# Optimization experiments

Measured on AMD Instinct MI355X. Metric: run time of the kernel, lower is better.

The kernel has to match this reference:

```python
import jax, jax.numpy as jnp
import numpy as np

EPS = float(np.finfo(np.float32).eps)

_base_x = np.array([[-1, 0, 1], [-2, 0, 2], [-1, 0, 1]], dtype=np.float32)
# 3D Sobel kernels (as in the torch module)
SOBEL_X_3D = np.stack([_base_x, 2 * _base_x, _base_x], axis=0)            # d-axis replication, x-grad along last axis
SOBEL_Y_3D = np.transpose(SOBEL_X_3D, (0, 2, 1))                          # rows/cols swapped -> y-grad
SOBEL_Z_3D = np.transpose(SOBEL_X_3D, (2, 1, 0))                          # z-grad along depth axis
# verify against explicit tensors from the source
assert np.array_equal(SOBEL_Y_3D[0], np.array([[-1, -2, -1], [0, 0, 0], [1, 2, 1]], dtype=np.float32))
assert np.array_equal(SOBEL_Z_3D[0], np.array([[-1, -2, -1], [-2, -4, -2], [-1, -2, -1]], dtype=np.float32))


def _sobel3d(image, kernel_np):
    # image: [B,1,D,H,W]; kernel: [3,3,3] -> OIDHW [1,1,3,3,3]
    k = jnp.asarray(kernel_np).reshape(1, 1, 3, 3, 3)
    return jax.lax.conv_general_dilated(
        image, k, window_strides=(1, 1, 1), padding='SAME',
        dimension_numbers=('NCDHW', 'OIDHW', 'NCDHW'))


def _normalized_gradient(image, mask, eta):
    # image, mask: [B,1,D,H,W]
    gx = _sobel3d(image, SOBEL_X_3D)
    gy = _sobel3d(image, SOBEL_Y_3D)
    gz = _sobel3d(image, SOBEL_Z_3D)
    grad = jnp.concatenate([gx, gy, gz], axis=1)          # [B,3,D,H,W]
    sq = jnp.sum(grad * grad, axis=1)                     # [B,D,H,W]
    norm = jnp.sqrt(sq + EPS)
    m = mask[:, 0]                                        # squeeze channel -> [B,D,H,W]
    dims = (1, 2, 3)
    auto_eps = eta / jnp.sum(m, axis=dims) * jnp.sum(norm * m, axis=dims)  # [B]
    auto_eps = auto_eps.reshape(-1, 1, 1, 1)
    denom = jnp.sqrt(sq + auto_eps ** 2 + EPS)            # [B,D,H,W]
    return grad / denom[:, None]                          # [B,3,D,H,W]


def setup_inputs() -> dict:
    key = jax.random.key(0)
    k1, k2 = jax.random.split(key)
    shape = (2, 1, 160, 160, 160)
    pred = jax.random.normal(k1, shape, dtype=jnp.float32)
    target = jax.random.normal(k2, shape, dtype=jnp.float32)
    mask = jnp.ones(shape, dtype=jnp.float32)
    return {"pred": pred, "target": target, "mask": mask}


def reference(pred, target, mask):
    eta = 1.0
    fixed_grad = jax.lax.stop_gradient(_normalized_gradient(target, mask, eta))
    warped_grad = _normalized_gradient(pred, mask, eta)
    inner = jnp.sum(fixed_grad * warped_grad, axis=1)     # [B,D,H,W]
    return 1.0 - jnp.mean(inner ** 2)
```

## Files before the change

kernel.cpp:

```cpp
#include <hip/hip_runtime.h>
#include <math.h>

#define DIM 160
#define NB 2
#define CHUNK 5
#define NCHZ (DIM / CHUNK)
#define NTHREADS 256
#define EPS_F 1.1920928955078125e-07f


__device__ __forceinline__ float4 ldv(const float* __restrict__ p, bool ok) {
  float4 r = make_float4(0.f, 0.f, 0.f, 0.f);
  if (ok) r = *(const float4*)p;
  return r;
}

__device__ __forceinline__ void plane_P(const float* __restrict__ img, int off0,
                                        bool zok, bool ym, bool yp, bool xl, bool xr,
                                        float (&P1)[4], float (&P2)[4], float (&P3)[4]) {
#pragma unroll
  for (int r = 0; r < 3; ++r) {
    const bool rv = zok && (r == 0 ? ym : (r == 2 ? yp : true));
    const int offr = off0 + (r - 1) * DIM;
    float4 L = ldv(img + offr - 4, rv && xl);
    float4 M = ldv(img + offr, rv);
    float4 R = ldv(img + offr + 4, rv && xr);
    float fm1 = L.w, f0 = M.x, f1 = M.y, f2 = M.z, f3 = M.w, f4 = R.x;
    float S[4], D[4];
    S[0] = fm1 + 2.f * f0 + f1;  D[0] = f1 - fm1;
    S[1] = f0 + 2.f * f1 + f2;   D[1] = f2 - f0;
    S[2] = f1 + 2.f * f2 + f3;   D[2] = f3 - f1;
    S[3] = f2 + 2.f * f3 + f4;   D[3] = f4 - f2;
    if (r == 0) {
#pragma unroll
      for (int j = 0; j < 4; ++j) { P1[j] = D[j]; P2[j] = -S[j]; P3[j] = S[j]; }
    } else if (r == 1) {
#pragma unroll
      for (int j = 0; j < 4; ++j) { P1[j] += 2.f * D[j]; P3[j] += 2.f * S[j]; }
    } else {
#pragma unroll
      for (int j = 0; j < 4; ++j) { P1[j] += D[j]; P2[j] += S[j]; P3[j] += S[j]; }
    }
  }
}

__global__ __launch_bounds__(NTHREADS)
void pass1_kernel(const float* __restrict__ pred, const float* __restrict__ tgt,
                  const float* __restrict__ mask, double* __restrict__ ws) {
  __shared__ float red[2][4];
  const int tid = threadIdx.x;
  const int tx = tid & 7, ty = tid >> 3;
  int bz = blockIdx.z;
  const int im = bz & 1; bz >>= 1;
  const int n = bz / NCHZ;
  const int zs = (bz % NCHZ) * CHUNK;
  const int xb = blockIdx.x * 32 + tx * 4;
  const int y = blockIdx.y * 32 + ty;
  const size_t base = (size_t)n * DIM * DIM * DIM;
  const float* img = (im == 0 ? pred : tgt) + base;
  const float* mb = mask + base;

  const bool xl = (xb >= 4), xr = (xb + 4 < DIM);
  const bool ym = (y >= 1), yp = (y <= DIM - 2);

  float OUT[2][3][4];
#pragma unroll
  for (int s = 0; s < 2; ++s)
#pragma unroll
    for (int f = 0; f < 3; ++f)
#pragma unroll
      for (int j = 0; j < 4; ++j) OUT[s][f][j] = 0.f;

  float am = 0.f, an = 0.f;

#pragma unroll
  for (int i = 0; i < CHUNK + 2; ++i) {
    const int z = zs - 1 + i;
    const bool zok = ((unsigned)z < DIM);
    const int off0 = (z * DIM + y) * DIM + xb;
    float P1[4], P2[4], P3[4];
    plane_P(img, off0, zok, ym, yp, xl, xr, P1, P2, P3);
    const int sA = i & 1, sB = sA ^ 1;
    if (i >= 2) {
      const int zo = z - 1;
      if (im == 0) {
        const float4 mv = *(const float4*)(mb + (zo * DIM + y) * DIM + xb);
        const float m4[4] = {mv.x, mv.y, mv.z, mv.w};
#pragma unroll
        for (int j = 0; j < 4; ++j) {
          float gx = OUT[sA][0][j] + P1[j];
          float gy = OUT[sA][1][j] + P2[j];
          float gz = OUT[sA][2][j] + P3[j];
          am += m4[j];
          an += sqrtf(gx * gx + gy * gy + gz * gz + EPS_F) * m4[j];
        }
      } else {
#pragma unroll
        for (int j = 0; j < 4; ++j) {
          float gx = OUT[sA][0][j] + P1[j];
          float gy = OUT[sA][1][j] + P2[j];
          float gz = OUT[sA][2][j] + P3[j];
          an += sqrtf(gx * gx + gy * gy + gz * gz + EPS_F);
        }
      }
    }
#pragma unroll
    for (int j = 0; j < 4; ++j) {
      OUT[sA][0][j] = P1[j];
      OUT[sA][1][j] = P2[j];
      OUT[sA][2][j] = -P3[j];
      OUT[sB][0][j] += 2.f * P1[j];
      OUT[sB][1][j] += 2.f * P2[j];
    }
  }

  float v0 = am, v1 = an;
#pragma unroll
  for (int off = 32; off > 0; off >>= 1) {
    v0 += __shfl_down(v0, off, 64);
    v1 += __shfl_down(v1, off, 64);
  }
  const int lane = tid & 63, wave = tid >> 6;
  if (lane == 0) { red[0][wave] = v0; red[1][wave] = v1; }
  __syncthreads();
  if (tid == 0) {
    if (im == 0) atomicAdd(&ws[0 + n], (double)(red[0][0] + red[0][1] + red[0][2] + red[0][3]));
    atomicAdd(&ws[2 + 2 * im + n], (double)(red[1][0] + red[1][1] + red[1][2] + red[1][3]));
  }
}

__global__ void compute_c_kernel(double* __restrict__ ws) {
  if (threadIdx.x == 0 && blockIdx.x == 0) {
    for (int n = 0; n < NB; ++n) {
      double inv_m = 1.0 / ws[0 + n];
      double ae_p = ws[2 + n] * inv_m;
      double ae_t = ws[4 + n] * inv_m;
      ws[8 + n] = ae_p * ae_p + (double)EPS_F;
      ws[10 + n] = ae_t * ae_t + (double)EPS_F;
    }
  }
}

__global__ __launch_bounds__(NTHREADS)
void pass2_kernel(const float* __restrict__ pred, const float* __restrict__ tgt,
                  double* __restrict__ ws) {
  __shared__ float red[4];
  const int tid = threadIdx.x;
  const int tx = tid & 7, ty = tid >> 3;
  const int bz = blockIdx.z;
  const int n = bz / NCHZ;
  const int zs = (bz % NCHZ) * CHUNK;
  const int xb = blockIdx.x * 32 + tx * 4;
  const int y = blockIdx.y * 32 + ty;
  const size_t base = (size_t)n * DIM * DIM * DIM;
  const float* pb = pred + base;
  const float* tb = tgt + base;

  const float cp = (float)ws[8 + n];
  const float ct = (float)ws[10 + n];

  const bool xl = (xb >= 4), xr = (xb + 4 < DIM);
  const bool ym = (y >= 1), yp = (y <= DIM - 2);

  float OUT[2][2][3][4];
#pragma unroll
  for (int s = 0; s < 2; ++s)
#pragma unroll
    for (int g = 0; g < 2; ++g)
#pragma unroll
      for (int f = 0; f < 3; ++f)
#pragma unroll
        for (int j = 0; j < 4; ++j) OUT[s][g][f][j] = 0.f;

  float acc = 0.f;

#pragma unroll
  for (int i = 0; i < CHUNK + 2; ++i) {
    const int z = zs - 1 + i;
    const bool zok = ((unsigned)z < DIM);
    const int off0 = (z * DIM + y) * DIM + xb;
    float P[2][3][4];
    plane_P(pb, off0, zok, ym, yp, xl, xr, P[0][0], P[0][1], P[0][2]);
    plane_P(tb, off0, zok, ym, yp, xl, xr, P[1][0], P[1][1], P[1][2]);
    const int sA = i & 1, sB = sA ^ 1;
    if (i >= 2) {
#pragma unroll
      for (int j = 0; j < 4; ++j) {
        float gpx = OUT[sA][0][0][j] + P[0][0][j];
        float gpy = OUT[sA][0][1][j] + P[0][1][j];
        float gpz = OUT[sA][0][2][j] + P[0][2][j];
        float gtx = OUT[sA][1][0][j] + P[1][0][j];
        float gty = OUT[sA][1][1][j] + P[1][1][j];
        float gtz = OUT[sA][1][2][j] + P[1][2][j];
        float sqp = gpx * gpx + gpy * gpy + gpz * gpz;
        float sqt = gtx * gtx + gty * gty + gtz * gtz;
        float dot = gpx * gtx + gpy * gty + gpz * gtz;
        float inner = dot * rsqrtf((sqp + cp) * (sqt + ct));
        acc += inner * inner;
      }
    }
#pragma unroll
    for (int g = 0; g < 2; ++g)
#pragma unroll
      for (int j = 0; j < 4; ++j) {
        OUT[sA][g][0][j] = P[g][0][j];
        OUT[sA][g][1][j] = P[g][1][j];
        OUT[sA][g][2][j] = -P[g][2][j];
        OUT[sB][g][0][j] += 2.f * P[g][0][j];
        OUT[sB][g][1][j] += 2.f * P[g][1][j];
      }
  }

#pragma unroll
  for (int off = 32; off > 0; off >>= 1) acc += __shfl_down(acc, off, 64);
  const int lane = tid & 63, wave = tid >> 6;
  if (lane == 0) red[wave] = acc;
  __syncthreads();
  if (tid == 0) atomicAdd(&ws[6], (double)(red[0] + red[1] + red[2] + red[3]));
}

__global__ void finalize_kernel(const double* __restrict__ ws, float* __restrict__ out) {
  if (threadIdx.x == 0 && blockIdx.x == 0) {
    double mean = ws[6] / ((double)NB * DIM * DIM * DIM);
    out[0] = (float)(1.0 - mean);
  }
}

extern "C" void kernel_launch(void* const* d_in, const int* in_sizes, int n_in,
                              void* d_out, int out_size, void* d_ws, size_t ws_size,
                              hipStream_t stream) {
  const float* pred = (const float*)d_in[0];
  const float* tgt = (const float*)d_in[1];
  const float* mask = (const float*)d_in[2];
  float* out = (float*)d_out;
  double* ws = (double*)d_ws;

  hipMemsetAsync(d_ws, 0, 16 * sizeof(double), stream);

  dim3 grid1(DIM / 32, DIM / 32, NCHZ * NB * 2);
  pass1_kernel<<<grid1, NTHREADS, 0, stream>>>(pred, tgt, mask, ws);
  compute_c_kernel<<<1, 64, 0, stream>>>(ws);
  dim3 grid2(DIM / 32, DIM / 32, NCHZ * NB);
  pass2_kernel<<<grid2, NTHREADS, 0, stream>>>(pred, tgt, ws);
  finalize_kernel<<<1, 64, 0, stream>>>(ws, out);
}
```

Measured before the change: 152.2 us.

## Stage z-planes through double-buffered LDS and fuse pred/target in pass1

Both passes now cooperatively load each z-plane tile with halo (34 rows by 44 floats, for pred and target) into a double-buffered shared-memory buffer, and compute the Sobel stencils from LDS instead of issuing nine overlapping global vector loads per thread. Boundary handling moves from predicated loads to clamped addresses plus multiplicative zero factors. Pass1 processes pred and target in the same block rather than in separate blocks, the z chunk doubles to 10, and the launch bounds request two blocks per CU. The aim is less redundant global/L2 traffic, at the cost of two barriers per plane, more registers and fewer blocks in the grid.

```diff
diff --git a/kernel.cpp b/kernel.cpp
--- a/kernel.cpp
+++ b/kernel.cpp
@@ -3,38 +3,83 @@
 
 #define DIM 160
 #define NB 2
-#define CHUNK 5
+#define CHUNK 10
 #define NCHZ (DIM / CHUNK)
 #define NTHREADS 256
 #define EPS_F 1.1920928955078125e-07f
 
-
-__device__ __forceinline__ float4 ldv(const float* __restrict__ p, bool ok) {
-  float4 r = make_float4(0.f, 0.f, 0.f, 0.f);
-  if (ok) r = *(const float4*)p;
-  return r;
-}
-
-__device__ __forceinline__ void plane_P(const float* __restrict__ img, int off0,
-                                        bool zok, bool ym, bool yp, bool xl, bool xr,
-                                        float (&P1)[4], float (&P2)[4], float (&P3)[4]) {
-#pragma unroll
-  for (int r = 0; r < 3; ++r) {
-    const bool rv = zok && (r == 0 ? ym : (r == 2 ? yp : true));
-    const int offr = off0 + (r - 1) * DIM;
-    float4 L = ldv(img + offr - 4, rv && xl);
-    float4 M = ldv(img + offr, rv);
-    float4 R = ldv(img + offr + 4, rv && xr);
-    float fm1 = L.w, f0 = M.x, f1 = M.y, f2 = M.z, f3 = M.w, f4 = R.x;
+#define CW 10
+#define RH 34
+#define LS 44
+#define PLANE_F (RH * LS)
+#define NCK (2 * RH * CW)
+
+typedef float v4f __attribute__((ext_vector_type(4)));
+
+__device__ __forceinline__ int imin(int a, int b) { return a < b ? a : b; }
+__device__ __forceinline__ int imax(int a, int b) { return a > b ? a : b; }
+
+
+struct Slot {
+  const float* srcb;
+  int ldsoff;
+  bool act;
+};
+
+__device__ __forceinline__ void make_slots(const float* __restrict__ pb,
+                                           const float* __restrict__ tb,
+                                           int x0, int y0, int tid, Slot (&sl)[3]) {
+#pragma unroll
+  for (int s = 0; s < 3; ++s) {
+    const int i = tid + NTHREADS * s;
+    sl[s].act = (i < NCK);
+    const int ii = sl[s].act ? i : 0;
+    const int img = ii / (RH * CW);
+    const int rem = ii - img * (RH * CW);
+    const int row = rem / CW, ch = rem - row * CW;
+    const int yc = imin(imax(y0 - 1 + row, 0), DIM - 1);
+    const int xc = imin(imax(x0 - 4 + 4 * ch, 0), DIM - 4);
+    sl[s].srcb = (img ? tb : pb) + yc * DIM + xc;
+    sl[s].ldsoff = img * PLANE_F + row * LS + 4 * ch;
+  }
+}
+
+__device__ __forceinline__ void stage_load(const Slot (&sl)[3], int z, v4f (&r)[3]) {
+  const int zoff = imin(imax(z, 0), DIM - 1) * DIM * DIM;
+#pragma unroll
+  for (int s = 0; s < 3; ++s)
+    if (sl[s].act) r[s] = *(const v4f*)(sl[s].srcb + zoff);
+}
+
+__device__ __forceinline__ void stage_write(float* __restrict__ buf,
+                                            const Slot (&sl)[3], const v4f (&r)[3]) {
+#pragma unroll
+  for (int s = 0; s < 3; ++s)
+    if (sl[s].act) *(v4f*)(buf + sl[s].ldsoff) = r[s];
+}
+
+__device__ __forceinline__ void compute_P_lds(const float* __restrict__ pl,
+                                              int tx, int ty,
+                                              float rf0, float rf1, float rf2,
+                                              float fxl, float fxr,
+                                              float (&P1)[4], float (&P2)[4], float (&P3)[4]) {
+#pragma unroll
+  for (int rr = 0; rr < 3; ++rr) {
+    const float rf = (rr == 0) ? rf0 : (rr == 1) ? rf1 : rf2;
+    const float* row = pl + (ty + rr) * LS + 4 * tx;
+    const v4f L = *(const v4f*)row;
+    const v4f M = *(const v4f*)(row + 4);
+    const v4f R = *(const v4f*)(row + 8);
+    const float fm1 = L.w * fxl, f0 = M.x, f1 = M.y, f2 = M.z, f3 = M.w, f4 = R.x * fxr;
     float S[4], D[4];
-    S[0] = fm1 + 2.f * f0 + f1;  D[0] = f1 - fm1;
-    S[1] = f0 + 2.f * f1 + f2;   D[1] = f2 - f0;
-    S[2] = f1 + 2.f * f2 + f3;   D[2] = f3 - f1;
-    S[3] = f2 + 2.f * f3 + f4;   D[3] = f4 - f2;
-    if (r == 0) {
+    S[0] = (fm1 + 2.f * f0 + f1) * rf;  D[0] = (f1 - fm1) * rf;
+    S[1] = (f0 + 2.f * f1 + f2) * rf;   D[1] = (f2 - f0) * rf;
+    S[2] = (f1 + 2.f * f2 + f3) * rf;   D[2] = (f3 - f1) * rf;
+    S[3] = (f2 + 2.f * f3 + f4) * rf;   D[3] = (f4 - f2) * rf;
+    if (rr == 0) {
 #pragma unroll
       for (int j = 0; j < 4; ++j) { P1[j] = D[j]; P2[j] = -S[j]; P3[j] = S[j]; }
-    } else if (r == 1) {
+    } else if (rr == 1) {
 #pragma unroll
       for (int j = 0; j < 4; ++j) { P1[j] += 2.f * D[j]; P3[j] += 2.f * S[j]; }
     } else {
@@ -44,88 +89,110 @@
   }
 }
 
-__global__ __launch_bounds__(NTHREADS)
+__global__ __launch_bounds__(NTHREADS, 2)
 void pass1_kernel(const float* __restrict__ pred, const float* __restrict__ tgt,
                   const float* __restrict__ mask, double* __restrict__ ws) {
-  __shared__ float red[2][4];
+  __shared__ float lds[2][2 * PLANE_F];
+  __shared__ float red[3][4];
   const int tid = threadIdx.x;
   const int tx = tid & 7, ty = tid >> 3;
-  int bz = blockIdx.z;
-  const int im = bz & 1; bz >>= 1;
-  const int n = bz / NCHZ;
-  const int zs = (bz % NCHZ) * CHUNK;
-  const int xb = blockIdx.x * 32 + tx * 4;
-  const int y = blockIdx.y * 32 + ty;
+  const int n = blockIdx.z / NCHZ;
+  const int zs = (blockIdx.z % NCHZ) * CHUNK;
+  const int x0 = blockIdx.x * 32, y0 = blockIdx.y * 32;
   const size_t base = (size_t)n * DIM * DIM * DIM;
-  const float* img = (im == 0 ? pred : tgt) + base;
+  const float* pb = pred + base;
+  const float* tb = tgt + base;
   const float* mb = mask + base;
-
-  const bool xl = (xb >= 4), xr = (xb + 4 < DIM);
-  const bool ym = (y >= 1), yp = (y <= DIM - 2);
-
-  float OUT[2][3][4];
+  const int x = x0 + 4 * tx, y = y0 + ty;
+
+  const float fxl = (x > 0) ? 1.f : 0.f;
+  const float fxr = (x + 4 < DIM) ? 1.f : 0.f;
+  const float fym = (y > 0) ? 1.f : 0.f;
+  const float fyp = (y < DIM - 1) ? 1.f : 0.f;
+
+  Slot sl[3];
+  make_slots(pb, tb, x0, y0, tid, sl);
+
+  float OUT[2][2][3][4];
 #pragma unroll
   for (int s = 0; s < 2; ++s)
 #pragma unroll
-    for (int f = 0; f < 3; ++f)
-#pragma unroll
-      for (int j = 0; j < 4; ++j) OUT[s][f][j] = 0.f;
-
-  float am = 0.f, an = 0.f;
-
-#pragma unroll
-  for (int i = 0; i < CHUNK + 2; ++i) {
+    for (int g = 0; g < 2; ++g)
+#pragma unroll
+      for (int f = 0; f < 3; ++f)
+#pragma unroll
+        for (int j = 0; j < 4; ++j) OUT[s][g][f][j] = 0.f;
+
+  float am = 0.f, anp = 0.f, ant = 0.f;
+  v4f stg[3];
+
+  stage_load(sl, zs - 1, stg);
+  stage_write(lds[0], sl, stg);
+  __syncthreads();
+
+#pragma unroll
+  for (int i = 0; i <= CHUNK + 1; ++i) {
     const int z = zs - 1 + i;
-    const bool zok = ((unsigned)z < DIM);
-    const int off0 = (z * DIM + y) * DIM + xb;
-    float P1[4], P2[4], P3[4];
-    plane_P(img, off0, zok, ym, yp, xl, xr, P1, P2, P3);
+    if (i <= CHUNK) stage_load(sl, zs + i, stg);
+
+    const float fz = ((unsigned)z < DIM) ? 1.f : 0.f;
+    const float* bufb = lds[i & 1];
+    float P[2][3][4];
+    compute_P_lds(bufb, tx, ty, fz * fym, fz, fz * fyp, fxl, fxr,
+                  P[0][0], P[0][1], P[0][2]);
+    compute_P_lds(bufb + PLANE_F, tx, ty, fz * fym, fz, fz * fyp, fxl, fxr,
+                  P[1][0], P[1][1], P[1][2]);
+
     const int sA = i & 1, sB = sA ^ 1;
     if (i >= 2) {
       const int zo = z - 1;
-      if (im == 0) {
-        const float4 mv = *(const float4*)(mb + (zo * DIM + y) * DIM + xb);
-        const float m4[4] = {mv.x, mv.y, mv.z, mv.w};
-#pragma unroll
-        for (int j = 0; j < 4; ++j) {
-          float gx = OUT[sA][0][j] + P1[j];
-          float gy = OUT[sA][1][j] + P2[j];
-          float gz = OUT[sA][2][j] + P3[j];
-          am += m4[j];
-          an += sqrtf(gx * gx + gy * gy + gz * gz + EPS_F) * m4[j];
-        }
-      } else {
-#pragma unroll
-        for (int j = 0; j < 4; ++j) {
-          float gx = OUT[sA][0][j] + P1[j];
-          float gy = OUT[sA][1][j] + P2[j];
-          float gz = OUT[sA][2][j] + P3[j];
-          an += sqrtf(gx * gx + gy * gy + gz * gz + EPS_F);
-        }
+      const v4f mv = *(const v4f*)(mb + (zo * DIM + y) * DIM + x);
+#pragma unroll
+      for (int j = 0; j < 4; ++j) {
+        const float mj = (j == 0) ? mv.x : (j == 1) ? mv.y : (j == 2) ? mv.z : mv.w;
+        float gpx = OUT[sA][0][0][j] + P[0][0][j];
+        float gpy = OUT[sA][0][1][j] + P[0][1][j];
+        float gpz = OUT[sA][0][2][j] + P[0][2][j];
+        float gtx = OUT[sA][1][0][j] + P[1][0][j];
+        float gty = OUT[sA][1][1][j] + P[1][1][j];
+        float gtz = OUT[sA][1][2][j] + P[1][2][j];
+        am += mj;
+        anp += sqrtf(gpx * gpx + gpy * gpy + gpz * gpz + EPS_F) * mj;
+        ant += sqrtf(gtx * gtx + gty * gty + gtz * gtz + EPS_F) * mj;
       }
     }
 #pragma unroll
-    for (int j = 0; j < 4; ++j) {
-      OUT[sA][0][j] = P1[j];
-      OUT[sA][1][j] = P2[j];
-      OUT[sA][2][j] = -P3[j];
-      OUT[sB][0][j] += 2.f * P1[j];
-      OUT[sB][1][j] += 2.f * P2[j];
-    }
-  }
-
-  float v0 = am, v1 = an;
+    for (int g = 0; g < 2; ++g)
+#pragma unroll
+      for (int j = 0; j < 4; ++j) {
+        OUT[sA][g][0][j] = P[g][0][j];
+        OUT[sA][g][1][j] = P[g][1][j];
+        OUT[sA][g][2][j] = -P[g][2][j];
+        OUT[sB][g][0][j] += 2.f * P[g][0][j];
+        OUT[sB][g][1][j] += 2.f * P[g][1][j];
+      }
+
+    if (i <= CHUNK) {
+      __syncthreads();
+      stage_write(lds[(i & 1) ^ 1], sl, stg);
+      __syncthreads();
+    }
+  }
+
+  float v0 = am, v1 = anp, v2 = ant;
 #pragma unroll
   for (int off = 32; off > 0; off >>= 1) {
     v0 += __shfl_down(v0, off, 64);
     v1 += __shfl_down(v1, off, 64);
+    v2 += __shfl_down(v2, off, 64);
   }
   const int lane = tid & 63, wave = tid >> 6;
-  if (lane == 0) { red[0][wave] = v0; red[1][wave] = v1; }
+  if (lane == 0) { red[0][wave] = v0; red[1][wave] = v1; red[2][wave] = v2; }
   __syncthreads();
   if (tid == 0) {
-    if (im == 0) atomicAdd(&ws[0 + n], (double)(red[0][0] + red[0][1] + red[0][2] + red[0][3]));
-    atomicAdd(&ws[2 + 2 * im + n], (double)(red[1][0] + red[1][1] + red[1][2] + red[1][3]));
+    atomicAdd(&ws[0 + n], (double)(red[0][0] + red[0][1] + red[0][2] + red[0][3]));
+    atomicAdd(&ws[2 + n], (double)(red[1][0] + red[1][1] + red[1][2] + red[1][3]));
+    atomicAdd(&ws[4 + n], (double)(red[2][0] + red[2][1] + red[2][2] + red[2][3]));
   }
 }
 
@@ -141,17 +208,16 @@
   }
 }
 
-__global__ __launch_bounds__(NTHREADS)
+__global__ __launch_bounds__(NTHREADS, 2)
 void pass2_kernel(const float* __restrict__ pred, const float* __restrict__ tgt,
                   double* __restrict__ ws) {
+  __shared__ float lds[2][2 * PLANE_F];
   __shared__ float red[4];
   const int tid = threadIdx.x;
   const int tx = tid & 7, ty = tid >> 3;
-  const int bz = blockIdx.z;
-  const int n = bz / NCHZ;
-  const int zs = (bz % NCHZ) * CHUNK;
-  const int xb = blockIdx.x * 32 + tx * 4;
-  const int y = blockIdx.y * 32 + ty;
+  const int n = blockIdx.z / NCHZ;
+  const int zs = (blockIdx.z % NCHZ) * CHUNK;
+  const int x0 = blockIdx.x * 32, y0 = blockIdx.y * 32;
   const size_t base = (size_t)n * DIM * DIM * DIM;
   const float* pb = pred + base;
   const float* tb = tgt + base;
@@ -159,8 +225,14 @@
   const float cp = (float)ws[8 + n];
   const float ct = (float)ws[10 + n];
 
-  const bool xl = (xb >= 4), xr = (xb + 4 < DIM);
-  const bool ym = (y >= 1), yp = (y <= DIM - 2);
+  const int x = x0 + 4 * tx, y = y0 + ty;
+  const float fxl = (x > 0) ? 1.f : 0.f;
+  const float fxr = (x + 4 < DIM) ? 1.f : 0.f;
+  const float fym = (y > 0) ? 1.f : 0.f;
+  const float fyp = (y < DIM - 1) ? 1.f : 0.f;
+
+  Slot sl[3];
+  make_slots(pb, tb, x0, y0, tid, sl);
 
   float OUT[2][2][3][4];
 #pragma unroll
@@ -173,15 +245,25 @@
         for (int j = 0; j < 4; ++j) OUT[s][g][f][j] = 0.f;
 
   float acc = 0.f;
-
-#pragma unroll
-  for (int i = 0; i < CHUNK + 2; ++i) {
+  v4f stg[3];
+
+  stage_load(sl, zs - 1, stg);
+  stage_write(lds[0], sl, stg);
+  __syncthreads();
+
+#pragma unroll
+  for (int i = 0; i <= CHUNK + 1; ++i) {
     const int z = zs - 1 + i;
-    const bool zok = ((unsigned)z < DIM);
-    const int off0 = (z * DIM + y) * DIM + xb;
+    if (i <= CHUNK) stage_load(sl, zs + i, stg);
+
+    const float fz = ((unsigned)z < DIM) ? 1.f : 0.f;
+    const float* bufb = lds[i & 1];
     float P[2][3][4];
-    plane_P(pb, off0, zok, ym, yp, xl, xr, P[0][0], P[0][1], P[0][2]);
-    plane_P(tb, off0, zok, ym, yp, xl, xr, P[1][0], P[1][1], P[1][2]);
+    compute_P_lds(bufb, tx, ty, fz * fym, fz, fz * fyp, fxl, fxr,
+                  P[0][0], P[0][1], P[0][2]);
+    compute_P_lds(bufb + PLANE_F, tx, ty, fz * fym, fz, fz * fyp, fxl, fxr,
+                  P[1][0], P[1][1], P[1][2]);
+
     const int sA = i & 1, sB = sA ^ 1;
     if (i >= 2) {
 #pragma unroll
@@ -209,6 +291,12 @@
         OUT[sB][g][0][j] += 2.f * P[g][0][j];
         OUT[sB][g][1][j] += 2.f * P[g][1][j];
       }
+
+    if (i <= CHUNK) {
+      __syncthreads();
+      stage_write(lds[(i & 1) ^ 1], sl, stg);
+      __syncthreads();
+    }
   }
 
 #pragma unroll
@@ -237,10 +325,9 @@
 
   hipMemsetAsync(d_ws, 0, 16 * sizeof(double), stream);
 
-  dim3 grid1(DIM / 32, DIM / 32, NCHZ * NB * 2);
-  pass1_kernel<<<grid1, NTHREADS, 0, stream>>>(pred, tgt, mask, ws);
+  dim3 grid(DIM / 32, DIM / 32, NCHZ * NB);
+  pass1_kernel<<<grid, NTHREADS, 0, stream>>>(pred, tgt, mask, ws);
   compute_c_kernel<<<1, 64, 0, stream>>>(ws);
-  dim3 grid2(DIM / 32, DIM / 32, NCHZ * NB);
-  pass2_kernel<<<grid2, NTHREADS, 0, stream>>>(pred, tgt, ws);
+  pass2_kernel<<<grid, NTHREADS, 0, stream>>>(pred, tgt, ws);
   finalize_kernel<<<1, 64, 0, stream>>>(ws, out);
 }
```

Result: slower. 262.5 us (+72.5%).

## Software-pipeline z-plane loads with clamped unconditional loads and scheduling barriers

Applied to the files above, without the earlier changes.

Replaces predicated boundary loads with clamped-address unconditional vector loads. Out-of-range values are zeroed by multiplying with float masks. Both passes now prefetch the next z-plane's 9 vector loads (and the mask) into register buffers before computing on the current plane. Sched barriers stop the compiler from reordering these, so memory latency should overlap with arithmetic. The cost is higher register pressure, and the fixed ordering may reduce occupancy or hurt scheduling.

```diff
diff --git a/kernel.cpp b/kernel.cpp
--- a/kernel.cpp
+++ b/kernel.cpp
@@ -8,29 +8,39 @@
 #define NTHREADS 256
 #define EPS_F 1.1920928955078125e-07f
 
-
-__device__ __forceinline__ float4 ldv(const float* __restrict__ p, bool ok) {
-  float4 r = make_float4(0.f, 0.f, 0.f, 0.f);
-  if (ok) r = *(const float4*)p;
-  return r;
-}
-
-__device__ __forceinline__ void plane_P(const float* __restrict__ img, int off0,
-                                        bool zok, bool ym, bool yp, bool xl, bool xr,
-                                        float (&P1)[4], float (&P2)[4], float (&P3)[4]) {
+typedef float v4f __attribute__((ext_vector_type(4)));
+
+#define SBAR() __builtin_amdgcn_sched_barrier(0)
+
+__device__ __forceinline__ int imin(int a, int b) { return a < b ? a : b; }
+__device__ __forceinline__ int imax(int a, int b) { return a > b ? a : b; }
+
+
+__device__ __forceinline__ void issue_plane(const float* __restrict__ img, int zoff,
+                                            int ro0, int ro1, int ro2,
+                                            int xL, int xM, int xR, v4f (&B)[9]) {
+  const float* r0 = img + zoff + ro0;
+  const float* r1 = img + zoff + ro1;
+  const float* r2 = img + zoff + ro2;
+  B[0] = *(const v4f*)(r0 + xL); B[1] = *(const v4f*)(r0 + xM); B[2] = *(const v4f*)(r0 + xR);
+  B[3] = *(const v4f*)(r1 + xL); B[4] = *(const v4f*)(r1 + xM); B[5] = *(const v4f*)(r1 + xR);
+  B[6] = *(const v4f*)(r2 + xL); B[7] = *(const v4f*)(r2 + xM); B[8] = *(const v4f*)(r2 + xR);
+}
+
+__device__ __forceinline__ void compute_P(const v4f (&B)[9],
+                                          float rf0, float rf1, float rf2,
+                                          float fxl, float fxr,
+                                          float (&P1)[4], float (&P2)[4], float (&P3)[4]) {
 #pragma unroll
   for (int r = 0; r < 3; ++r) {
-    const bool rv = zok && (r == 0 ? ym : (r == 2 ? yp : true));
-    const int offr = off0 + (r - 1) * DIM;
-    float4 L = ldv(img + offr - 4, rv && xl);
-    float4 M = ldv(img + offr, rv);
-    float4 R = ldv(img + offr + 4, rv && xr);
-    float fm1 = L.w, f0 = M.x, f1 = M.y, f2 = M.z, f3 = M.w, f4 = R.x;
+    const float rf = (r == 0) ? rf0 : (r == 1) ? rf1 : rf2;
+    const v4f L = B[r * 3 + 0], M = B[r * 3 + 1], R = B[r * 3 + 2];
+    const float fm1 = L.w * fxl, f0 = M.x, f1 = M.y, f2 = M.z, f3 = M.w, f4 = R.x * fxr;
     float S[4], D[4];
-    S[0] = fm1 + 2.f * f0 + f1;  D[0] = f1 - fm1;
-    S[1] = f0 + 2.f * f1 + f2;   D[1] = f2 - f0;
-    S[2] = f1 + 2.f * f2 + f3;   D[2] = f3 - f1;
-    S[3] = f2 + 2.f * f3 + f4;   D[3] = f4 - f2;
+    S[0] = (fm1 + 2.f * f0 + f1) * rf;  D[0] = (f1 - fm1) * rf;
+    S[1] = (f0 + 2.f * f1 + f2) * rf;   D[1] = (f2 - f0) * rf;
+    S[2] = (f1 + 2.f * f2 + f3) * rf;   D[2] = (f3 - f1) * rf;
+    S[3] = (f2 + 2.f * f3 + f4) * rf;   D[3] = (f4 - f2) * rf;
     if (r == 0) {
 #pragma unroll
       for (int j = 0; j < 4; ++j) { P1[j] = D[j]; P2[j] = -S[j]; P3[j] = S[j]; }
@@ -60,8 +70,15 @@
   const float* img = (im == 0 ? pred : tgt) + base;
   const float* mb = mask + base;
 
-  const bool xl = (xb >= 4), xr = (xb + 4 < DIM);
-  const bool ym = (y >= 1), yp = (y <= DIM - 2);
+  const float fxl = (xb >= 4) ? 1.f : 0.f;
+  const float fxr = (xb + 4 < DIM) ? 1.f : 0.f;
+  const float fym = (y >= 1) ? 1.f : 0.f;
+  const float fyp = (y <= DIM - 2) ? 1.f : 0.f;
+
+  const int ro0 = imax(y - 1, 0) * DIM;
+  const int ro1 = y * DIM;
+  const int ro2 = imin(y + 1, DIM - 1) * DIM;
+  const int xL = imax(xb - 4, 0), xM = xb, xR = imin(xb + 4, DIM - 4);
 
   float OUT[2][3][4];
 #pragma unroll
@@ -72,45 +89,55 @@
       for (int j = 0; j < 4; ++j) OUT[s][f][j] = 0.f;
 
   float am = 0.f, an = 0.f;
-
-#pragma unroll
-  for (int i = 0; i < CHUNK + 2; ++i) {
+  v4f BUF[2][9];
+  v4f MV[2];
+  MV[0] = (v4f)(0.f); MV[1] = (v4f)(0.f);
+
+  issue_plane(img, imin(imax(zs - 1, 0), DIM - 1) * DIM * DIM,
+              ro0, ro1, ro2, xL, xM, xR, BUF[0]);
+
+#pragma unroll
+  for (int i = 0; i <= CHUNK + 1; ++i) {
     const int z = zs - 1 + i;
-    const bool zok = ((unsigned)z < DIM);
-    const int off0 = (z * DIM + y) * DIM + xb;
-    float P1[4], P2[4], P3[4];
-    plane_P(img, off0, zok, ym, yp, xl, xr, P1, P2, P3);
+    if (i <= CHUNK)
+      issue_plane(img, imin(zs + i, DIM - 1) * DIM * DIM,
+                  ro0, ro1, ro2, xL, xM, xR, BUF[(i + 1) & 1]);
+    if (im == 0 && i >= 1 && i <= CHUNK)
+      MV[(i + 1) & 1] = *(const v4f*)(mb + ((zs + i - 1) * DIM + y) * DIM + xb);
+    SBAR();
+    const float fz = ((unsigned)z < DIM) ? 1.f : 0.f;
+    float P1a[4], P2a[4], P3a[4];
+    compute_P(BUF[i & 1], fz * fym, fz, fz * fyp, fxl, fxr, P1a, P2a, P3a);
     const int sA = i & 1, sB = sA ^ 1;
     if (i >= 2) {
-      const int zo = z - 1;
       if (im == 0) {
-        const float4 mv = *(const float4*)(mb + (zo * DIM + y) * DIM + xb);
-        const float m4[4] = {mv.x, mv.y, mv.z, mv.w};
+        const v4f mv = MV[i & 1];
 #pragma unroll
         for (int j = 0; j < 4; ++j) {
-          float gx = OUT[sA][0][j] + P1[j];
-          float gy = OUT[sA][1][j] + P2[j];
-          float gz = OUT[sA][2][j] + P3[j];
-          am += m4[j];
-          an += sqrtf(gx * gx + gy * gy + gz * gz + EPS_F) * m4[j];
+          const float mj = (j == 0) ? mv.x : (j == 1) ? mv.y : (j == 2) ? mv.z : mv.w;
+          float gx = OUT[sA][0][j] + P1a[j];
+          float gy = OUT[sA][1][j] + P2a[j];
+          float gz = OUT[sA][2][j] + P3a[j];
+          am += mj;
+          an += sqrtf(gx * gx + gy * gy + gz * gz + EPS_F) * mj;
         }
       } else {
 #pragma unroll
         for (int j = 0; j < 4; ++j) {
-          float gx = OUT[sA][0][j] + P1[j];
-          float gy = OUT[sA][1][j] + P2[j];
-          float gz = OUT[sA][2][j] + P3[j];
+          float gx = OUT[sA][0][j] + P1a[j];
+          float gy = OUT[sA][1][j] + P2a[j];
+          float gz = OUT[sA][2][j] + P3a[j];
           an += sqrtf(gx * gx + gy * gy + gz * gz + EPS_F);
         }
       }
     }
 #pragma unroll
     for (int j = 0; j < 4; ++j) {
-      OUT[sA][0][j] = P1[j];
-      OUT[sA][1][j] = P2[j];
-      OUT[sA][2][j] = -P3[j];
-      OUT[sB][0][j] += 2.f * P1[j];
-      OUT[sB][1][j] += 2.f * P2[j];
+      OUT[sA][0][j] = P1a[j];
+      OUT[sA][1][j] = P2a[j];
+      OUT[sA][2][j] = -P3a[j];
+      OUT[sB][0][j] += 2.f * P1a[j];
+      OUT[sB][1][j] += 2.f * P2a[j];
     }
   }
 
@@ -159,8 +186,15 @@
   const float cp = (float)ws[8 + n];
   const float ct = (float)ws[10 + n];
 
-  const bool xl = (xb >= 4), xr = (xb + 4 < DIM);
-  const bool ym = (y >= 1), yp = (y <= DIM - 2);
+  const float fxl = (xb >= 4) ? 1.f : 0.f;
+  const float fxr = (xb + 4 < DIM) ? 1.f : 0.f;
+  const float fym = (y >= 1) ? 1.f : 0.f;
+  const float fyp = (y <= DIM - 2) ? 1.f : 0.f;
+
+  const int ro0 = imax(y - 1, 0) * DIM;
+  const int ro1 = y * DIM;
+  const int ro2 = imin(y + 1, DIM - 1) * DIM;
+  const int xL = imax(xb - 4, 0), xM = xb, xR = imin(xb + 4, DIM - 4);
 
   float OUT[2][2][3][4];
 #pragma unroll
@@ -173,25 +207,39 @@
         for (int j = 0; j < 4; ++j) OUT[s][g][f][j] = 0.f;
 
   float acc = 0.f;
-
-#pragma unroll
-  for (int i = 0; i < CHUNK + 2; ++i) {
+  v4f PBUF[9], TBUF[9];
+
+  {
+    const int z0off = imin(imax(zs - 1, 0), DIM - 1) * DIM * DIM;
+    issue_plane(pb, z0off, ro0, ro1, ro2, xL, xM, xR, PBUF);
+    issue_plane(tb, z0off, ro0, ro1, ro2, xL, xM, xR, TBUF);
+  }
+
+#pragma unroll
+  for (int i = 0; i <= CHUNK + 1; ++i) {
     const int z = zs - 1 + i;
-    const bool zok = ((unsigned)z < DIM);
-    const int off0 = (z * DIM + y) * DIM + xb;
-    float P[2][3][4];
-    plane_P(pb, off0, zok, ym, yp, xl, xr, P[0][0], P[0][1], P[0][2]);
-    plane_P(tb, off0, zok, ym, yp, xl, xr, P[1][0], P[1][1], P[1][2]);
+    const float fz = ((unsigned)z < DIM) ? 1.f : 0.f;
+    const int znoff = imin(zs + i, DIM - 1) * DIM * DIM;
+
+    float Pp1[4], Pp2[4], Pp3[4];
+    compute_P(PBUF, fz * fym, fz, fz * fyp, fxl, fxr, Pp1, Pp2, Pp3);
+    if (i <= CHUNK) issue_plane(pb, znoff, ro0, ro1, ro2, xL, xM, xR, PBUF);
+    SBAR();
+    float Pt1[4], Pt2[4], Pt3[4];
+    compute_P(TBUF, fz * fym, fz, fz * fyp, fxl, fxr, Pt1, Pt2, Pt3);
+    if (i <= CHUNK) issue_plane(tb, znoff, ro0, ro1, ro2, xL, xM, xR, TBUF);
+    SBAR();
+
     const int sA = i & 1, sB = sA ^ 1;
     if (i >= 2) {
 #pragma unroll
       for (int j = 0; j < 4; ++j) {
-        float gpx = OUT[sA][0][0][j] + P[0][0][j];
-        float gpy = OUT[sA][0][1][j] + P[0][1][j];
-        float gpz = OUT[sA][0][2][j] + P[0][2][j];
-        float gtx = OUT[sA][1][0][j] + P[1][0][j];
-        float gty = OUT[sA][1][1][j] + P[1][1][j];
-        float gtz = OUT[sA][1][2][j] + P[1][2][j];
+        float gpx = OUT[sA][0][0][j] + Pp1[j];
+        float gpy = OUT[sA][0][1][j] + Pp2[j];
+        float gpz = OUT[sA][0][2][j] + Pp3[j];
+        float gtx = OUT[sA][1][0][j] + Pt1[j];
+        float gty = OUT[sA][1][1][j] + Pt2[j];
+        float gtz = OUT[sA][1][2][j] + Pt3[j];
         float sqp = gpx * gpx + gpy * gpy + gpz * gpz;
         float sqt = gtx * gtx + gty * gty + gtz * gtz;
         float dot = gpx * gtx + gpy * gty + gpz * gtz;
@@ -200,15 +248,18 @@
       }
     }
 #pragma unroll
-    for (int g = 0; g < 2; ++g)
-#pragma unroll
-      for (int j = 0; j < 4; ++j) {
-        OUT[sA][g][0][j] = P[g][0][j];
-        OUT[sA][g][1][j] = P[g][1][j];
-        OUT[sA][g][2][j] = -P[g][2][j];
-        OUT[sB][g][0][j] += 2.f * P[g][0][j];
-        OUT[sB][g][1][j] += 2.f * P[g][1][j];
-      }
+    for (int j = 0; j < 4; ++j) {
+      OUT[sA][0][0][j] = Pp1[j];
+      OUT[sA][0][1][j] = Pp2[j];
+      OUT[sA][0][2][j] = -Pp3[j];
+      OUT[sB][0][0][j] += 2.f * Pp1[j];
+      OUT[sB][0][1][j] += 2.f * Pp2[j];
+      OUT[sA][1][0][j] = Pt1[j];
+      OUT[sA][1][1][j] = Pt2[j];
+      OUT[sA][1][2][j] = -Pt3[j];
+      OUT[sB][1][0][j] += 2.f * Pt1[j];
+      OUT[sB][1][1][j] += 2.f * Pt2[j];
+    }
   }
 
 #pragma unroll
```

Result: faster. 146.2 us (-3.9%).
